# Optimization experiments

Hardware: AMD Instinct MI355X
Metric: run time of the kernel (lower is better)

## Reference

```python
import jax, jax.numpy as jnp
import numpy as np

K, B, T, Y, X, HY, HX = 8, 64, 128, 128, 64, 256, 256


def sparsemax(z):
    # projection onto the simplex along last axis
    zs = jnp.flip(jnp.sort(z, axis=-1), axis=-1)
    k = jnp.arange(1, z.shape[-1] + 1, dtype=z.dtype)
    cssv = jnp.cumsum(zs, axis=-1) - 1.0
    cond = k * zs > cssv
    kz = jnp.sum(cond, axis=-1, keepdims=True)
    tau = jnp.take_along_axis(cssv, kz - 1, axis=-1) / kz.astype(z.dtype)
    return jnp.maximum(z - tau, 0.0)


def rnn_relu(x, Wih, Whh, bih, bhh, h0):
    # batch-first relu RNN: x [B,T,D] -> h [B,T,H]
    xW = jnp.einsum('btd,hd->bth', x, Wih) + bih
    h0b = jnp.broadcast_to(h0, (x.shape[0], h0.shape[0]))
    def step(h, xt):
        h = jax.nn.relu(xt + h @ Whh.T + bhh)
        return h, h
    _, hs = jax.lax.scan(step, h0b, jnp.swapaxes(xW, 0, 1))
    return jnp.swapaxes(hs, 0, 1)


def setup_inputs() -> dict:
    ks = jax.random.split(jax.random.key(0), 32)
    s = 0.05
    p = lambda k, sh: jax.random.normal(k, sh, jnp.float32) * s
    return {
        'data': jax.random.normal(ks[0], (B, T, Y), jnp.float32),
        'eps_qx': jax.random.normal(ks[1], (K, B, T, X), jnp.float32),
        'eps_z': jax.random.normal(ks[2], (T, B, K), jnp.float32),
        'eps_x': jax.random.normal(ks[3], (T, B, X), jnp.float32),
        'y_Wih': p(ks[4], (K, HY, Y)), 'y_Whh': p(ks[5], (K, HY, HY)),
        'y_bih': p(ks[6], (K, HY)), 'y_bhh': p(ks[7], (K, HY)),
        'y_h0': jnp.zeros((K, HY), jnp.float32),
        'y_Wmu': p(ks[8], (K, X, HY)), 'y_bmu': p(ks[9], (K, X)),
        'x_Wih': p(ks[10], (K, HX, X)), 'x_Whh': p(ks[11], (K, HX, HX)),
        'x_bih': p(ks[12], (K, HX)), 'x_bhh': p(ks[13], (K, HX)),
        'x_h0': jnp.zeros((K, HX), jnp.float32),
        'ds_W': p(ks[14], (HX, K * HX)), 'ds_b': p(ks[15], (HX,)),
        'cb_W1': p(ks[16], (HX, K)), 'cb_b1': p(ks[17], (HX,)),
        'cb_W2': p(ks[18], (K, HX)), 'cb_b2': p(ks[19], (K,)),
        'z_q0': jnp.zeros((K,), jnp.float32),
    }


def _forward(data, eps_qx, eps_z, eps_x, y_Wih, y_Whh, y_bih, y_bhh, y_h0,
             y_Wmu, y_bmu, x_Wih, x_Whh, x_bih, x_bhh, x_h0,
             ds_W, ds_b, cb_W1, cb_b1, cb_W2, cb_b2, z_q0):
    Bn, Tn, _ = data.shape
    Kn = z_q0.shape[0]
    vr = jax.vmap(rnn_relu, in_axes=(None, 0, 0, 0, 0, 0))
    vrx = jax.vmap(rnn_relu, in_axes=(0, 0, 0, 0, 0, 0))
    # per-state LDM inference over reversed y: q(x^k_{1:T} | y_{1:T})
    data_rev = jnp.flip(data, axis=1)
    h_y = jnp.flip(vr(data_rev, y_Wih, y_Whh, y_bih, y_bhh, y_h0), axis=2)  # [K,B,T,HY]
    q_x_mu = jnp.einsum('kbth,kxh->kbtx', h_y, y_Wmu) + y_bmu[:, None, None, :]
    q_x_logvar = jnp.zeros_like(q_x_mu)
    q_x = q_x_mu + eps_qx  # sigma = exp(0.5*0) = 1
    # per-state summary RNN over reversed q_x samples
    q_x_rev = jnp.flip(q_x, axis=2)
    h_x = jnp.flip(vrx(q_x_rev, x_Wih, x_Whh, x_bih, x_bhh, x_h0), axis=2)  # [K,B,T,HX]
    summary = jnp.transpose(h_x, (1, 2, 0, 3)).reshape(Bn, Tn, -1)  # [B,T,K*HX]
    xs = summary @ ds_W.T + ds_b  # downsampler -> [B,T,HX]
    xs_t_all = jnp.swapaxes(xs, 0, 1)              # [T,B,HX]
    mu_t_all = jnp.transpose(q_x_mu, (2, 1, 0, 3))  # [T,B,K,X]
    z0 = jnp.broadcast_to(z_q0, (Bn, Kn))
    def step(z_prev, inp):
        xs_t, mu_t, ez, ex = inp
        h = z_prev @ cb_W1.T + cb_b1 + xs_t          # combiner hidden
        z_mu = h @ cb_W2.T + cb_b2                   # logits mu (logvar=0)
        z_t = z_mu + ez
        w = sparsemax(z_t)                            # [B,K] gating
        x_t = jnp.einsum('bk,bkx->bx', w, mu_t) + ex  # mixture reparam (sigma=1)
        return z_t, (x_t, z_t, z_mu)
    _, (x_s, z_s, z_l) = jax.lax.scan(step, z0, (xs_t_all, mu_t_all, eps_z, eps_x))
    x_sample = jnp.swapaxes(x_s, 0, 1)
    z_sample = jnp.swapaxes(z_s, 0, 1)
    z_logits = jnp.swapaxes(z_l, 0, 1)
    return (x_sample, q_x_mu, q_x_logvar, z_sample, z_logits)


def reference(data, eps_qx, eps_z, eps_x, y_Wih, y_Whh, y_bih, y_bhh, y_h0,
              y_Wmu, y_bmu, x_Wih, x_Whh, x_bih, x_bhh, x_h0,
              ds_W, ds_b, cb_W1, cb_b1, cb_W2, cb_b2, z_q0):
    return _forward(data, eps_qx, eps_z, eps_x, y_Wih, y_Whh, y_bih, y_bhh, y_h0,
                    y_Wmu, y_bmu, x_Wih, x_Whh, x_bih, x_bhh, x_h0,
                    ds_W, ds_b, cb_W1, cb_b1, cb_W2, cb_b2, z_q0)
```

## Files before the change

### kernel.cpp

```cpp
#include <hip/hip_runtime.h>

#define Kc 8
#define Bc 64
#define Tc 128
#define Yc 128
#define Xc 64
#define Hc 256
#define Rc 8192

typedef unsigned short u16;
typedef unsigned int u32;
typedef __attribute__((ext_vector_type(8))) short short8;
typedef __attribute__((ext_vector_type(4))) float f32x4;
typedef __attribute__((ext_vector_type(2))) unsigned int u32x2;

#define OFF_DATA 0L
#define OFF_YWIH 1048576L
#define OFF_YWHH 1310720L
#define OFF_YWMU 1835008L
#define OFF_XWIH 1966080L
#define OFF_XWHH 2097152L
#define OFF_M2   2621440L
#define OFF_QXF  2654208L
#define OFF_BUF1 6848512L
#define U16_BYTES 80805888L
#define FO_YB 0L
#define FO_XB 2048L
#define FO_CB 4096L
#define FO_A2 4112L
#define FO_CP 8192L
#define FO_C  532480L
#define FO_W  598016L


#define O_XS  0L
#define O_QMU 524288L
#define O_QLV 4718592L
#define O_ZS  8912896L
#define O_ZL  8978432L

__device__ __forceinline__ u16 f2bf(float f) {
  union { float f; u32 u; } v; v.f = f;
  u32 u = v.u;
  return (u16)((u + 0x7FFFu + ((u >> 16) & 1u)) >> 16);
}
__device__ __forceinline__ float bitsf(u32 u) {
  union { u32 u; float f; } v; v.u = u; return v.f;
}
__device__ __forceinline__ u32 cvt_pk(float lo, float hi) {
  u32 r;
  asm("v_cvt_pk_bf16_f32 %0, %1, %2" : "=v"(r) : "v"(lo), "v"(hi));
  return r;
}
__device__ __forceinline__ f32x4 mfma16(short8 a, short8 b, f32x4 c) {
  return __builtin_amdgcn_mfma_f32_16x16x32_bf16(a, b, c, 0, 0, 0);
}

__global__ void k_prep(const float* __restrict__ data, const float* __restrict__ yWih,
                       const float* __restrict__ yWhh, const float* __restrict__ yWmu,
                       const float* __restrict__ xWih, const float* __restrict__ xWhh,
                       const float* __restrict__ ybih, const float* __restrict__ ybhh,
                       const float* __restrict__ xbih, const float* __restrict__ xbhh,
                       u16* __restrict__ W, float* __restrict__ F, float* __restrict__ out)
{
  long tid = (long)blockIdx.x * blockDim.x + threadIdx.x;
  long stride = (long)gridDim.x * blockDim.x;
  for (long i = tid; i < 1048576L; i += stride) W[OFF_DATA + i] = f2bf(data[i]);
  for (long i = tid; i < 262144L;  i += stride) W[OFF_YWIH + i] = f2bf(yWih[i]);
  for (long i = tid; i < 524288L;  i += stride) W[OFF_YWHH + i] = f2bf(yWhh[i]);
  for (long i = tid; i < 131072L;  i += stride) W[OFF_YWMU + i] = f2bf(yWmu[i]);
  for (long i = tid; i < 131072L;  i += stride) W[OFF_XWIH + i] = f2bf(xWih[i]);
  for (long i = tid; i < 524288L;  i += stride) W[OFF_XWHH + i] = f2bf(xWhh[i]);
  for (long i = tid; i < 2048L;    i += stride) F[FO_YB + i] = ybih[i] + ybhh[i];
  for (long i = tid; i < 2048L;    i += stride) F[FO_XB + i] = xbih[i] + xbhh[i];
  for (long i = tid; i < 4194304L; i += stride) out[O_QLV + i] = 0.0f;
}

__global__ void k_prep2(const float* __restrict__ dsW, const float* __restrict__ dsb,
                        const float* __restrict__ W1, const float* __restrict__ b1,
                        const float* __restrict__ W2, const float* __restrict__ b2,
                        u16* __restrict__ W, float* __restrict__ F)
{
  if (blockIdx.x < 128) {
    long i = (long)blockIdx.x * 256 + threadIdx.x;
    int k2 = (int)(i >> 11), ki = (int)(i & 2047);
    float s = 0.0f;
    if (k2 < 8) {
      for (int j = 0; j < 256; ++j) s += W2[k2 * 256 + j] * dsW[(long)j * 2048 + ki];
    }
    W[OFF_M2 + i] = f2bf(s);
  } else {
    int t = threadIdx.x;
    if (t < 64) {
      int k2 = t >> 3, k1 = t & 7;
      float s = 0.0f;
      for (int j = 0; j < 256; ++j) s += W2[k2 * 256 + j] * W1[j * 8 + k1];
      F[FO_A2 + t] = s;
    } else if (t < 80) {
      int k2 = t - 64;
      float s = 0.0f;
      if (k2 < 8) {
        for (int j = 0; j < 256; ++j) s += W2[k2 * 256 + j] * (dsb[j] + b1[j]);
        s += b2[k2];
      }
      F[FO_CB + k2] = s;
    }
  }
}

__global__ __launch_bounds__(256) void k_g1(const u16* __restrict__ W, const float* __restrict__ F,
                                            u16* __restrict__ buf)
{
  const int k = blockIdx.y, bs = blockIdx.x >> 5, t0 = (blockIdx.x & 31) * 4;
  const int tid = threadIdx.x, wv = tid >> 6, l = tid & 63, lr = l & 15, lk = l >> 4;
  const int b0 = bs * 16;
  short8 Af[4][4];
  const u16* Ak = W + OFF_YWIH + (long)k * 32768;
#pragma unroll
  for (int nt = 0; nt < 4; ++nt)
#pragma unroll
    for (int kk = 0; kk < 4; ++kk)
      Af[nt][kk] = *(const short8*)(Ak + (long)(wv * 64 + nt * 16 + lr) * 128 + kk * 32 + lk * 8);
  f32x4 bias[4];
#pragma unroll
  for (int nt = 0; nt < 4; ++nt)
    bias[nt] = *(const f32x4*)&F[FO_YB + k * 256 + wv * 64 + nt * 16 + lk * 4];
  int roff[4];
#pragma unroll
  for (int nt = 0; nt < 4; ++nt)
    roff[nt] = (wv * 2 + (nt >> 1)) * 512 + ((nt & 1) * 2 + (lk >> 1)) * 128 + lr * 8 + (lk & 1) * 4;

  for (int ti = 0; ti < 4; ++ti) {
    int t = t0 + ti;
    f32x4 acc[4] = {bias[0], bias[1], bias[2], bias[3]};
    const u16* Brow = W + OFF_DATA + ((long)(b0 + lr) * 128 + t) * 128 + lk * 8;
#pragma unroll
    for (int kk = 0; kk < 4; ++kk) {
      short8 b = *(const short8*)(Brow + kk * 32);
      acc[0] = mfma16(Af[0][kk], b, acc[0]);
      acc[1] = mfma16(Af[1][kk], b, acc[1]);
      acc[2] = mfma16(Af[2][kk], b, acc[2]);
      acc[3] = mfma16(Af[3][kk], b, acc[3]);
    }
    u16* tb = buf + ((long)(k * 4 + bs) * 128 + t) * 4096;
#pragma unroll
    for (int nt = 0; nt < 4; ++nt) {
      u32 d0 = cvt_pk(acc[nt][0], acc[nt][1]);
      u32 d1 = cvt_pk(acc[nt][2], acc[nt][3]);
      *(u32x2*)(tb + roff[nt]) = (u32x2){d0, d1};
    }
  }
}

#define RNNY_STEP(T_, XW_, PIN_, POUT_)                                       \
  {                                                                           \
    f32x4 acc[4];                                                             \
    _Pragma("unroll")                                                         \
    for (int nt = 0; nt < 4; ++nt) {                                          \
      u32 w0 = XW_[nt * 2], w1 = XW_[nt * 2 + 1];                             \
      acc[nt][0] = bitsf(w0 << 16);                                           \
      acc[nt][1] = bitsf(w0 & 0xffff0000u);                                   \
      acc[nt][2] = bitsf(w1 << 16);                                           \
      acc[nt][3] = bitsf(w1 & 0xffff0000u);                                   \
    }                                                                         \
    if ((T_) >= 2) {                                                          \
      _Pragma("unroll")                                                       \
      for (int nt = 0; nt < 4; ++nt) {                                        \
        u32x2 v = *(const u32x2*)(tb0 + (long)((T_) - 2) * 4096 + roff[nt]);  \
        XW_[nt * 2] = v.x; XW_[nt * 2 + 1] = v.y;                             \
      }                                                                       \
    }                                                                         \
    _Pragma("unroll")                                                         \
    for (int kk = 0; kk < 8; ++kk) {                                          \
      short8 b = *(const short8*)&hlds[PIN_][kk * 512 + fro];                 \
      acc[0] = mfma16(Bf[0][kk], b, acc[0]);                                  \
      acc[1] = mfma16(Bf[1][kk], b, acc[1]);                                  \
      acc[2] = mfma16(Bf[2][kk], b, acc[2]);                                  \
      acc[3] = mfma16(Bf[3][kk], b, acc[3]);                                  \
    }                                                                         \
    u16* tb = tb0 + (long)(T_) * 4096;                                        \
    _Pragma("unroll")                                                         \
    for (int nt = 0; nt < 4; ++nt) {                                          \
      float f0 = fmaxf(acc[nt][0], 0.0f), f1 = fmaxf(acc[nt][1], 0.0f);       \
      float f2 = fmaxf(acc[nt][2], 0.0f), f3 = fmaxf(acc[nt][3], 0.0f);       \
      u32x2 d = (u32x2){cvt_pk(f0, f1), cvt_pk(f2, f3)};                      \
      *(u32x2*)&hlds[POUT_][roff[nt]] = d;                                    \
      *(u32x2*)(tb + roff[nt]) = d;                                           \
    }                                                                         \
    asm volatile("s_waitcnt lgkmcnt(0)" ::: "memory");                        \
    __builtin_amdgcn_s_barrier();                                             \
    __builtin_amdgcn_sched_barrier(0);                                        \
  }

__global__ __launch_bounds__(256, 1) void k_rnnY(u16* __restrict__ buf,
                                                 const u16* __restrict__ Whh,
                                                 const float* __restrict__ h0)
{
  const int k = blockIdx.y, bs = blockIdx.x;
  const int tid = threadIdx.x, wv = tid >> 6, l = tid & 63, lr = l & 15, lk = l >> 4;
  const int fro = lk * 128 + lr * 8;
  __shared__ __align__(16) u16 hlds[2][4096];

  short8 Bf[4][8];
  const u16* Wk = Whh + (long)k * 65536;
#pragma unroll
  for (int nt = 0; nt < 4; ++nt)
#pragma unroll
    for (int kk = 0; kk < 8; ++kk)
      Bf[nt][kk] = *(const short8*)(Wk + (long)(wv * 64 + nt * 16 + lr) * 256 + kk * 32 + lk * 8);

  for (int i = tid; i < 4096; i += 256) {
    int n = (i >> 9) * 32 + ((i >> 7) & 3) * 8 + (i & 7);
    hlds[0][i] = f2bf(h0[k * 256 + n]);
  }

  u16* tb0 = buf + (long)(k * 4 + bs) * 128 * 4096;
  int roff[4];
#pragma unroll
  for (int nt = 0; nt < 4; ++nt)
    roff[nt] = (wv * 2 + (nt >> 1)) * 512 + ((nt & 1) * 2 + (lk >> 1)) * 128 + lr * 8 + (lk & 1) * 4;

  u32 xwA[8], xwB[8];
#pragma unroll
  for (int nt = 0; nt < 4; ++nt) {
    u32x2 vA = *(const u32x2*)(tb0 + (long)(Tc - 1) * 4096 + roff[nt]);
    xwA[nt * 2] = vA.x; xwA[nt * 2 + 1] = vA.y;
    u32x2 vB = *(const u32x2*)(tb0 + (long)(Tc - 2) * 4096 + roff[nt]);
    xwB[nt * 2] = vB.x; xwB[nt * 2 + 1] = vB.y;
  }
  __syncthreads();

  for (int t = Tc - 1; t >= 1; t -= 2) {
    RNNY_STEP(t, xwA, 0, 1);
    RNNY_STEP(t - 1, xwB, 1, 0);
  }
}

__global__ __launch_bounds__(256) void k_g2(const u16* __restrict__ W, const u16* __restrict__ hy,
                                            const float* __restrict__ bmu, const float* __restrict__ eps,
                                            float* __restrict__ out, u16* __restrict__ qxf)
{
  const int k = blockIdx.y, bs = blockIdx.x >> 5, t0 = (blockIdx.x & 31) * 4;
  const int tid = threadIdx.x, wv = tid >> 6, l = tid & 63, lr = l & 15, lk = l >> 4;
  const int b0 = bs * 16, x0 = wv * 16;
  short8 Af[8];
  const u16* Ak = W + OFF_YWMU + (long)k * 16384;
#pragma unroll
  for (int kk = 0; kk < 8; ++kk)
    Af[kk] = *(const short8*)(Ak + (long)(x0 + lr) * 256 + kk * 32 + lk * 8);
  f32x4 bias = *(const f32x4*)&bmu[k * 64 + x0 + lk * 4];
  const int qoff = (wv >> 1) * 512 + ((wv & 1) * 2 + (lk >> 1)) * 128 + lr * 8 + (lk & 1) * 4;

  for (int ti = 0; ti < 4; ++ti) {
    int t = t0 + ti;
    const u16* tb = hy + ((long)(k * 4 + bs) * 128 + t) * 4096 + lk * 128 + lr * 8;
    f32x4 a0 = bias, a1 = (f32x4){0.f, 0.f, 0.f, 0.f};
#pragma unroll
    for (int kk = 0; kk < 8; kk += 2) {
      short8 bA = *(const short8*)(tb + kk * 512);
      short8 bB = *(const short8*)(tb + (kk + 1) * 512);
      a0 = mfma16(Af[kk], bA, a0);
      a1 = mfma16(Af[kk + 1], bB, a1);
    }
    f32x4 mu = a0 + a1;
    long idx = ((long)k * Rc + (b0 + lr) * 128 + t) * 64 + x0 + lk * 4;
    *(f32x4*)&out[O_QMU + idx] = mu;
    f32x4 e = *(const f32x4*)&eps[idx];
    f32x4 q = mu + e;
    *(u32x2*)(qxf + ((long)(k * 4 + bs) * 128 + t) * 1024 + qoff) =
        (u32x2){cvt_pk(q[0], q[1]), cvt_pk(q[2], q[3])};
  }
}

#define RNNX_STEP(T_, QC_, PIN_, POUT_)                                       \
  {                                                                           \
    short8 q0 = QC_[0], q1 = QC_[1];                                          \
    if ((T_) >= 2) {                                                          \
      QC_[0] = *(const short8*)(qb0 + (long)((T_) - 2) * 1024 + fro);         \
      QC_[1] = *(const short8*)(qb0 + (long)((T_) - 2) * 1024 + 512 + fro);   \
    }                                                                         \
    f32x4 acc[4] = {xbias[0], xbias[1], xbias[2], xbias[3]};                  \
    f32x4 cacc = (f32x4){0.f, 0.f, 0.f, 0.f};                                 \
    _Pragma("unroll")                                                         \
    for (int kk = 0; kk < 8; ++kk) {                                          \
      short8 b = *(const short8*)&hlds[PIN_][kk * 512 + fro];                 \
      acc[0] = mfma16(Bf[0][kk], b, acc[0]);                                  \
      acc[1] = mfma16(Bf[1][kk], b, acc[1]);                                  \
      acc[2] = mfma16(Bf[2][kk], b, acc[2]);                                  \
      acc[3] = mfma16(Bf[3][kk], b, acc[3]);                                  \
      if (wv == 0) cacc = mfma16(Mf[kk], b, cacc);                            \
    }                                                                         \
    acc[0] = mfma16(IhX[0][0], q0, acc[0]);                                   \
    acc[1] = mfma16(IhX[1][0], q0, acc[1]);                                   \
    acc[2] = mfma16(IhX[2][0], q0, acc[2]);                                   \
    acc[3] = mfma16(IhX[3][0], q0, acc[3]);                                   \
    acc[0] = mfma16(IhX[0][1], q1, acc[0]);                                   \
    acc[1] = mfma16(IhX[1][1], q1, acc[1]);                                   \
    acc[2] = mfma16(IhX[2][1], q1, acc[2]);                                   \
    acc[3] = mfma16(IhX[3][1], q1, acc[3]);                                   \
    if (wv == 0 && (T_) < Tc - 1 && lk < 2)                                   \
      *(f32x4*)&cp[((long)(b0 + lr) * Tc + (T_) + 1) * 8 + lk * 4] = cacc;    \
    _Pragma("unroll")                                                         \
    for (int nt = 0; nt < 4; ++nt) {                                          \
      float f0 = fmaxf(acc[nt][0], 0.0f), f1 = fmaxf(acc[nt][1], 0.0f);       \
      float f2 = fmaxf(acc[nt][2], 0.0f), f3 = fmaxf(acc[nt][3], 0.0f);       \
      *(u32x2*)&hlds[POUT_][roff[nt]] = (u32x2){cvt_pk(f0, f1), cvt_pk(f2, f3)}; \
    }                                                                         \
    asm volatile("s_waitcnt lgkmcnt(0)" ::: "memory");                        \
    __builtin_amdgcn_s_barrier();                                             \
    __builtin_amdgcn_sched_barrier(0);                                        \
  }

__global__ __launch_bounds__(256, 1) void k_rnnX(const u16* __restrict__ W,
                                                 const float* __restrict__ F,
                                                 const u16* __restrict__ qxf,
                                                 const float* __restrict__ h0,
                                                 float* __restrict__ cpart)
{
  const int k = blockIdx.y, bs = blockIdx.x, b0 = bs * 16;
  const int tid = threadIdx.x, wv = tid >> 6, l = tid & 63, lr = l & 15, lk = l >> 4;
  const int fro = lk * 128 + lr * 8;
  __shared__ __align__(16) u16 hlds[2][4096];

  short8 Bf[4][8];
  short8 IhX[4][2];
  short8 Mf[8];
  {
    const u16* Wk = W + OFF_XWHH + (long)k * 65536;
    const u16* Ik = W + OFF_XWIH + (long)k * 16384;
    const u16* Mk = W + OFF_M2 + (long)k * 256;
#pragma unroll
    for (int nt = 0; nt < 4; ++nt) {
#pragma unroll
      for (int kk = 0; kk < 8; ++kk)
        Bf[nt][kk] = *(const short8*)(Wk + (long)(wv * 64 + nt * 16 + lr) * 256 + kk * 32 + lk * 8);
#pragma unroll
      for (int kk = 0; kk < 2; ++kk)
        IhX[nt][kk] = *(const short8*)(Ik + (long)(wv * 64 + nt * 16 + lr) * 64 + kk * 32 + lk * 8);
    }
#pragma unroll
    for (int kk = 0; kk < 8; ++kk)
      Mf[kk] = *(const short8*)(Mk + (long)lr * 2048 + kk * 32 + lk * 8);
  }
  f32x4 xbias[4];
#pragma unroll
  for (int nt = 0; nt < 4; ++nt)
    xbias[nt] = *(const f32x4*)&F[FO_XB + k * 256 + wv * 64 + nt * 16 + lk * 4];
  int roff[4];
#pragma unroll
  for (int nt = 0; nt < 4; ++nt)
    roff[nt] = (wv * 2 + (nt >> 1)) * 512 + ((nt & 1) * 2 + (lk >> 1)) * 128 + lr * 8 + (lk & 1) * 4;

  for (int i = tid; i < 4096; i += 256) {
    int n = (i >> 9) * 32 + ((i >> 7) & 3) * 8 + (i & 7);
    hlds[0][i] = f2bf(h0[k * 256 + n]);
  }

  const u16* qb0 = qxf + (long)(k * 4 + bs) * 128 * 1024;
  float* cp = cpart + (long)k * Rc * 8;

  short8 qA[2], qB[2];
#pragma unroll
  for (int kk = 0; kk < 2; ++kk) {
    qA[kk] = *(const short8*)(qb0 + (long)(Tc - 1) * 1024 + kk * 512 + fro);
    qB[kk] = *(const short8*)(qb0 + (long)(Tc - 2) * 1024 + kk * 512 + fro);
  }
  __syncthreads();

  for (int t = Tc - 1; t >= 1; t -= 2) {
    RNNX_STEP(t, qA, 0, 1);
    RNNX_STEP(t - 1, qB, 1, 0);
  }
  if (wv == 0) {
    f32x4 cacc = (f32x4){0.f, 0.f, 0.f, 0.f};
#pragma unroll
    for (int kk = 0; kk < 8; ++kk) {
      short8 b = *(const short8*)&hlds[0][kk * 512 + fro];
      cacc = mfma16(Mf[kk], b, cacc);
    }
    if (lk < 2)
      *(f32x4*)&cp[((long)(b0 + lr) * Tc) * 8 + lk * 4] = cacc;
  }
}

__global__ void k_csum(const float* __restrict__ cpart, const float* __restrict__ F,
                       float* __restrict__ cbuf)
{
  int i = blockIdx.x * 256 + threadIdx.x;
  float s = F[FO_CB + (i & 7)];
#pragma unroll
  for (int k = 0; k < 8; ++k) s += cpart[(long)k * 65536 + i];
  cbuf[i] = s;
}

#define CASD(a, b) { float _hi = fmaxf(a, b), _lo = fminf(a, b); a = _hi; b = _lo; }
__global__ __launch_bounds__(256) void k_zchain(const float* __restrict__ F, const float* __restrict__ cbuf,
                                                const float* __restrict__ eps_z, const float* __restrict__ zq0,
                                                float* __restrict__ out, float* __restrict__ wbuf)
{
  const int wv = threadIdx.x >> 6, l = threadIdx.x & 63;
  const int b = blockIdx.x * 4 + wv;
  __shared__ float cl[4][1024];
  __shared__ float el[4][1024];
  for (int i = l; i < 1024; i += 64) cl[wv][i] = cbuf[(long)b * 1024 + i];
  for (int i = l; i < 1024; i += 64) {
    int t = i >> 3, kk = i & 7;
    el[wv][i] = eps_z[(long)t * (Bc * Kc) + b * 8 + kk];
  }
  float a2 = F[FO_A2 + l];
  __syncthreads();

  float z = zq0[l & 7];
  for (int t = 0; t < Tc; ++t) {
    float p = a2 * z;
    p += __shfl_xor(p, 1, 64);
    p += __shfl_xor(p, 2, 64);
    p += __shfl_xor(p, 4, 64);
    float zmu_l = __shfl(p, (l & 7) * 8, 64);
    float zl = zmu_l + cl[wv][t * 8 + (l & 7)];
    float zt = zl + el[wv][t * 8 + (l & 7)];

    float v0 = __shfl(zt, 0, 64), v1 = __shfl(zt, 1, 64), v2 = __shfl(zt, 2, 64), v3 = __shfl(zt, 3, 64);
    float v4 = __shfl(zt, 4, 64), v5 = __shfl(zt, 5, 64), v6 = __shfl(zt, 6, 64), v7 = __shfl(zt, 7, 64);
    CASD(v0, v1); CASD(v2, v3); CASD(v4, v5); CASD(v6, v7);
    CASD(v0, v2); CASD(v1, v3); CASD(v4, v6); CASD(v5, v7);
    CASD(v1, v2); CASD(v5, v6);
    CASD(v0, v4); CASD(v1, v5); CASD(v2, v6); CASD(v3, v7);
    CASD(v2, v4); CASD(v3, v5);
    CASD(v1, v2); CASD(v3, v4); CASD(v5, v6);
    float s0 = v0, s1 = s0 + v1, s2 = s1 + v2, s3 = s2 + v3;
    float s4 = s3 + v4, s5 = s4 + v5, s6 = s5 + v6, s7 = s6 + v7;
    int kz = 1;
    kz += (2.0f * v1 > s1 - 1.0f) ? 1 : 0;
    kz += (3.0f * v2 > s2 - 1.0f) ? 1 : 0;
    kz += (4.0f * v3 > s3 - 1.0f) ? 1 : 0;
    kz += (5.0f * v4 > s4 - 1.0f) ? 1 : 0;
    kz += (6.0f * v5 > s5 - 1.0f) ? 1 : 0;
    kz += (7.0f * v6 > s6 - 1.0f) ? 1 : 0;
    kz += (8.0f * v7 > s7 - 1.0f) ? 1 : 0;
    float csel = s0 - 1.0f;
    csel = (kz > 1) ? s1 - 1.0f : csel;
    csel = (kz > 2) ? s2 - 1.0f : csel;
    csel = (kz > 3) ? s3 - 1.0f : csel;
    csel = (kz > 4) ? s4 - 1.0f : csel;
    csel = (kz > 5) ? s5 - 1.0f : csel;
    csel = (kz > 6) ? s6 - 1.0f : csel;
    csel = (kz > 7) ? s7 - 1.0f : csel;
    float tau = csel / (float)kz;
    float wk = fmaxf(zt - tau, 0.0f);

    if (l < 8) {
      long r = (long)b * Tc + t;
      out[O_ZL + r * 8 + l] = zl;
      out[O_ZS + r * 8 + l] = zt;
      wbuf[r * 8 + l] = wk;
    }
    z = zt;
  }
}

__global__ void k_xsample(const float* __restrict__ wbuf, const float* __restrict__ eps_x,
                          float* __restrict__ out)
{
  long idx = (long)blockIdx.x * 256 + threadIdx.x;
  if (idx >= (long)Rc * Xc) return;
  long r = idx >> 6;
  int x = (int)(idx & 63);
  long b = r >> 7;
  long t = r & 127;
  float s = eps_x[(t * Bc + b) * 64 + x];
#pragma unroll
  for (int k = 0; k < 8; ++k)
    s += wbuf[r * 8 + k] * out[O_QMU + ((long)k * Rc + r) * 64 + x];
  out[O_XS + idx] = s;
}

extern "C" void kernel_launch(void* const* d_in, const int* in_sizes, int n_in,
                              void* d_out, int out_size, void* d_ws, size_t ws_size,
                              hipStream_t stream) {
  (void)in_sizes; (void)n_in; (void)out_size; (void)ws_size;
  const float* data   = (const float*)d_in[0];
  const float* eps_qx = (const float*)d_in[1];
  const float* eps_z  = (const float*)d_in[2];
  const float* eps_x  = (const float*)d_in[3];
  const float* yWih   = (const float*)d_in[4];
  const float* yWhh   = (const float*)d_in[5];
  const float* ybih   = (const float*)d_in[6];
  const float* ybhh   = (const float*)d_in[7];
  const float* yh0    = (const float*)d_in[8];
  const float* yWmu   = (const float*)d_in[9];
  const float* ybmu   = (const float*)d_in[10];
  const float* xWih   = (const float*)d_in[11];
  const float* xWhh   = (const float*)d_in[12];
  const float* xbih   = (const float*)d_in[13];
  const float* xbhh   = (const float*)d_in[14];
  const float* xh0    = (const float*)d_in[15];
  const float* dsW    = (const float*)d_in[16];
  const float* dsb    = (const float*)d_in[17];
  const float* cbW1   = (const float*)d_in[18];
  const float* cbb1   = (const float*)d_in[19];
  const float* cbW2   = (const float*)d_in[20];
  const float* cbb2   = (const float*)d_in[21];
  const float* zq0    = (const float*)d_in[22];

  u16*   W = (u16*)d_ws;
  float* F = (float*)((char*)d_ws + U16_BYTES);
  float* out = (float*)d_out;

  hipLaunchKernelGGL(k_prep, dim3(1024), dim3(256), 0, stream,
                     data, yWih, yWhh, yWmu, xWih, xWhh, ybih, ybhh, xbih, xbhh, W, F, out);
  hipLaunchKernelGGL(k_prep2, dim3(129), dim3(256), 0, stream,
                     dsW, dsb, cbW1, cbb1, cbW2, cbb2, W, F);
  hipLaunchKernelGGL(k_g1, dim3(128, 8), dim3(256), 0, stream, W, F, W + OFF_BUF1);
  hipLaunchKernelGGL(k_rnnY, dim3(4, 8), dim3(256), 0, stream, W + OFF_BUF1, W + OFF_YWHH, yh0);
  hipLaunchKernelGGL(k_g2, dim3(128, 8), dim3(256), 0, stream,
                     W, W + OFF_BUF1, ybmu, eps_qx, out, W + OFF_QXF);
  hipLaunchKernelGGL(k_rnnX, dim3(4, 8), dim3(256), 0, stream,
                     W, F, W + OFF_QXF, xh0, F + FO_CP);
  hipLaunchKernelGGL(k_csum, dim3(256), dim3(256), 0, stream, F + FO_CP, F, F + FO_C);
  hipLaunchKernelGGL(k_zchain, dim3(16), dim3(256), 0, stream, F, F + FO_C, eps_z, zq0, out, F + FO_W);
  hipLaunchKernelGGL(k_xsample, dim3(2048), dim3(256), 0, stream, F + FO_W, eps_x, out);
}
```

Measured before the change: 328.6 us.

## Use 8 waves per block in recurrent RNN kernels and fuse csum into zchain

Both sequential RNN kernels now run 512 threads (8 waves) per block, and each wave owns 32 hidden units instead of 64. That halves the MFMA chain each wave issues per serial timestep, which shortens the latency-bound recurrence. The separate k_csum kernel is removed and its partial-sum reduction is folded into k_zchain's load phase, saving one launch. In exchange there are more waves in each barrier, and the zchain prologue does more global reads.

```diff
diff --git a/kernel.cpp b/kernel.cpp
--- a/kernel.cpp
+++ b/kernel.cpp
@@ -29,7 +29,6 @@
 #define FO_CB 4096L
 #define FO_A2 4112L
 #define FO_CP 8192L
-#define FO_C  532480L
 #define FO_W  598016L
 
 
@@ -154,45 +153,37 @@
 
 #define RNNY_STEP(T_, XW_, PIN_, POUT_)                                       \
   {                                                                           \
-    f32x4 acc[4];                                                             \
-    _Pragma("unroll")                                                         \
-    for (int nt = 0; nt < 4; ++nt) {                                          \
-      u32 w0 = XW_[nt * 2], w1 = XW_[nt * 2 + 1];                             \
-      acc[nt][0] = bitsf(w0 << 16);                                           \
-      acc[nt][1] = bitsf(w0 & 0xffff0000u);                                   \
-      acc[nt][2] = bitsf(w1 << 16);                                           \
-      acc[nt][3] = bitsf(w1 & 0xffff0000u);                                   \
-    }                                                                         \
+    f32x4 acc0, acc1;                                                         \
+    { u32 w0 = XW_[0], w1 = XW_[1];                                           \
+      acc0[0] = bitsf(w0 << 16); acc0[1] = bitsf(w0 & 0xffff0000u);           \
+      acc0[2] = bitsf(w1 << 16); acc0[3] = bitsf(w1 & 0xffff0000u); }         \
+    { u32 w0 = XW_[2], w1 = XW_[3];                                           \
+      acc1[0] = bitsf(w0 << 16); acc1[1] = bitsf(w0 & 0xffff0000u);           \
+      acc1[2] = bitsf(w1 << 16); acc1[3] = bitsf(w1 & 0xffff0000u); }         \
     if ((T_) >= 2) {                                                          \
-      _Pragma("unroll")                                                       \
-      for (int nt = 0; nt < 4; ++nt) {                                        \
-        u32x2 v = *(const u32x2*)(tb0 + (long)((T_) - 2) * 4096 + roff[nt]);  \
-        XW_[nt * 2] = v.x; XW_[nt * 2 + 1] = v.y;                             \
-      }                                                                       \
+      u32x2 v0 = *(const u32x2*)(tb0 + (long)((T_) - 2) * 4096 + roff[0]);    \
+      u32x2 v1 = *(const u32x2*)(tb0 + (long)((T_) - 2) * 4096 + roff[1]);    \
+      XW_[0] = v0.x; XW_[1] = v0.y; XW_[2] = v1.x; XW_[3] = v1.y;             \
     }                                                                         \
     _Pragma("unroll")                                                         \
     for (int kk = 0; kk < 8; ++kk) {                                          \
       short8 b = *(const short8*)&hlds[PIN_][kk * 512 + fro];                 \
-      acc[0] = mfma16(Bf[0][kk], b, acc[0]);                                  \
-      acc[1] = mfma16(Bf[1][kk], b, acc[1]);                                  \
-      acc[2] = mfma16(Bf[2][kk], b, acc[2]);                                  \
-      acc[3] = mfma16(Bf[3][kk], b, acc[3]);                                  \
+      acc0 = mfma16(Bf[0][kk], b, acc0);                                      \
+      acc1 = mfma16(Bf[1][kk], b, acc1);                                      \
     }                                                                         \
     u16* tb = tb0 + (long)(T_) * 4096;                                        \
-    _Pragma("unroll")                                                         \
-    for (int nt = 0; nt < 4; ++nt) {                                          \
-      float f0 = fmaxf(acc[nt][0], 0.0f), f1 = fmaxf(acc[nt][1], 0.0f);       \
-      float f2 = fmaxf(acc[nt][2], 0.0f), f3 = fmaxf(acc[nt][3], 0.0f);       \
-      u32x2 d = (u32x2){cvt_pk(f0, f1), cvt_pk(f2, f3)};                      \
-      *(u32x2*)&hlds[POUT_][roff[nt]] = d;                                    \
-      *(u32x2*)(tb + roff[nt]) = d;                                           \
-    }                                                                         \
+    { u32x2 d = (u32x2){cvt_pk(fmaxf(acc0[0], 0.f), fmaxf(acc0[1], 0.f)),     \
+                        cvt_pk(fmaxf(acc0[2], 0.f), fmaxf(acc0[3], 0.f))};    \
+      *(u32x2*)&hlds[POUT_][roff[0]] = d; *(u32x2*)(tb + roff[0]) = d; }      \
+    { u32x2 d = (u32x2){cvt_pk(fmaxf(acc1[0], 0.f), fmaxf(acc1[1], 0.f)),     \
+                        cvt_pk(fmaxf(acc1[2], 0.f), fmaxf(acc1[3], 0.f))};    \
+      *(u32x2*)&hlds[POUT_][roff[1]] = d; *(u32x2*)(tb + roff[1]) = d; }      \
     asm volatile("s_waitcnt lgkmcnt(0)" ::: "memory");                        \
     __builtin_amdgcn_s_barrier();                                             \
     __builtin_amdgcn_sched_barrier(0);                                        \
   }
 
-__global__ __launch_bounds__(256, 1) void k_rnnY(u16* __restrict__ buf,
+__global__ __launch_bounds__(512, 1) void k_rnnY(u16* __restrict__ buf,
                                                  const u16* __restrict__ Whh,
                                                  const float* __restrict__ h0)
 {
@@ -201,32 +192,33 @@
   const int fro = lk * 128 + lr * 8;
   __shared__ __align__(16) u16 hlds[2][4096];
 
-  short8 Bf[4][8];
+  short8 Bf[2][8];
   const u16* Wk = Whh + (long)k * 65536;
 #pragma unroll
-  for (int nt = 0; nt < 4; ++nt)
+  for (int nt = 0; nt < 2; ++nt)
 #pragma unroll
     for (int kk = 0; kk < 8; ++kk)
-      Bf[nt][kk] = *(const short8*)(Wk + (long)(wv * 64 + nt * 16 + lr) * 256 + kk * 32 + lk * 8);
-
-  for (int i = tid; i < 4096; i += 256) {
+      Bf[nt][kk] = *(const short8*)(Wk + (long)(wv * 32 + nt * 16 + lr) * 256 + kk * 32 + lk * 8);
+
+  for (int i = tid; i < 4096; i += 512) {
     int n = (i >> 9) * 32 + ((i >> 7) & 3) * 8 + (i & 7);
     hlds[0][i] = f2bf(h0[k * 256 + n]);
   }
 
   u16* tb0 = buf + (long)(k * 4 + bs) * 128 * 4096;
-  int roff[4];
-#pragma unroll
-  for (int nt = 0; nt < 4; ++nt)
-    roff[nt] = (wv * 2 + (nt >> 1)) * 512 + ((nt & 1) * 2 + (lk >> 1)) * 128 + lr * 8 + (lk & 1) * 4;
-
-  u32 xwA[8], xwB[8];
-#pragma unroll
-  for (int nt = 0; nt < 4; ++nt) {
-    u32x2 vA = *(const u32x2*)(tb0 + (long)(Tc - 1) * 4096 + roff[nt]);
-    xwA[nt * 2] = vA.x; xwA[nt * 2 + 1] = vA.y;
-    u32x2 vB = *(const u32x2*)(tb0 + (long)(Tc - 2) * 4096 + roff[nt]);
-    xwB[nt * 2] = vB.x; xwB[nt * 2 + 1] = vB.y;
+  int roff[2];
+#pragma unroll
+  for (int nt = 0; nt < 2; ++nt)
+    roff[nt] = wv * 512 + (nt * 2 + (lk >> 1)) * 128 + lr * 8 + (lk & 1) * 4;
+
+  u32 xwA[4], xwB[4];
+  {
+    u32x2 a0 = *(const u32x2*)(tb0 + (long)(Tc - 1) * 4096 + roff[0]);
+    u32x2 a1 = *(const u32x2*)(tb0 + (long)(Tc - 1) * 4096 + roff[1]);
+    xwA[0] = a0.x; xwA[1] = a0.y; xwA[2] = a1.x; xwA[3] = a1.y;
+    u32x2 b0v = *(const u32x2*)(tb0 + (long)(Tc - 2) * 4096 + roff[0]);
+    u32x2 b1v = *(const u32x2*)(tb0 + (long)(Tc - 2) * 4096 + roff[1]);
+    xwB[0] = b0v.x; xwB[1] = b0v.y; xwB[2] = b1v.x; xwB[3] = b1v.y;
   }
   __syncthreads();
 
@@ -279,39 +271,33 @@
       QC_[0] = *(const short8*)(qb0 + (long)((T_) - 2) * 1024 + fro);         \
       QC_[1] = *(const short8*)(qb0 + (long)((T_) - 2) * 1024 + 512 + fro);   \
     }                                                                         \
-    f32x4 acc[4] = {xbias[0], xbias[1], xbias[2], xbias[3]};                  \
+    f32x4 acc0 = xbias[0], acc1 = xbias[1];                                   \
     f32x4 cacc = (f32x4){0.f, 0.f, 0.f, 0.f};                                 \
     _Pragma("unroll")                                                         \
     for (int kk = 0; kk < 8; ++kk) {                                          \
       short8 b = *(const short8*)&hlds[PIN_][kk * 512 + fro];                 \
-      acc[0] = mfma16(Bf[0][kk], b, acc[0]);                                  \
-      acc[1] = mfma16(Bf[1][kk], b, acc[1]);                                  \
-      acc[2] = mfma16(Bf[2][kk], b, acc[2]);                                  \
-      acc[3] = mfma16(Bf[3][kk], b, acc[3]);                                  \
+      acc0 = mfma16(Bf[0][kk], b, acc0);                                      \
+      acc1 = mfma16(Bf[1][kk], b, acc1);                                      \
       if (wv == 0) cacc = mfma16(Mf[kk], b, cacc);                            \
     }                                                                         \
-    acc[0] = mfma16(IhX[0][0], q0, acc[0]);                                   \
-    acc[1] = mfma16(IhX[1][0], q0, acc[1]);                                   \
-    acc[2] = mfma16(IhX[2][0], q0, acc[2]);                                   \
-    acc[3] = mfma16(IhX[3][0], q0, acc[3]);                                   \
-    acc[0] = mfma16(IhX[0][1], q1, acc[0]);                                   \
-    acc[1] = mfma16(IhX[1][1], q1, acc[1]);                                   \
-    acc[2] = mfma16(IhX[2][1], q1, acc[2]);                                   \
-    acc[3] = mfma16(IhX[3][1], q1, acc[3]);                                   \
+    acc0 = mfma16(IhX[0][0], q0, acc0);                                       \
+    acc1 = mfma16(IhX[1][0], q0, acc1);                                       \
+    acc0 = mfma16(IhX[0][1], q1, acc0);                                       \
+    acc1 = mfma16(IhX[1][1], q1, acc1);                                       \
     if (wv == 0 && (T_) < Tc - 1 && lk < 2)                                   \
       *(f32x4*)&cp[((long)(b0 + lr) * Tc + (T_) + 1) * 8 + lk * 4] = cacc;    \
-    _Pragma("unroll")                                                         \
-    for (int nt = 0; nt < 4; ++nt) {                                          \
-      float f0 = fmaxf(acc[nt][0], 0.0f), f1 = fmaxf(acc[nt][1], 0.0f);       \
-      float f2 = fmaxf(acc[nt][2], 0.0f), f3 = fmaxf(acc[nt][3], 0.0f);       \
-      *(u32x2*)&hlds[POUT_][roff[nt]] = (u32x2){cvt_pk(f0, f1), cvt_pk(f2, f3)}; \
-    }                                                                         \
+    { u32x2 d = (u32x2){cvt_pk(fmaxf(acc0[0], 0.f), fmaxf(acc0[1], 0.f)),     \
+                        cvt_pk(fmaxf(acc0[2], 0.f), fmaxf(acc0[3], 0.f))};    \
+      *(u32x2*)&hlds[POUT_][roff[0]] = d; }                                   \
+    { u32x2 d = (u32x2){cvt_pk(fmaxf(acc1[0], 0.f), fmaxf(acc1[1], 0.f)),     \
+                        cvt_pk(fmaxf(acc1[2], 0.f), fmaxf(acc1[3], 0.f))};    \
+      *(u32x2*)&hlds[POUT_][roff[1]] = d; }                                   \
     asm volatile("s_waitcnt lgkmcnt(0)" ::: "memory");                        \
     __builtin_amdgcn_s_barrier();                                             \
     __builtin_amdgcn_sched_barrier(0);                                        \
   }
 
-__global__ __launch_bounds__(256, 1) void k_rnnX(const u16* __restrict__ W,
+__global__ __launch_bounds__(512, 1) void k_rnnX(const u16* __restrict__ W,
                                                  const float* __restrict__ F,
                                                  const u16* __restrict__ qxf,
                                                  const float* __restrict__ h0,
@@ -322,36 +308,36 @@
   const int fro = lk * 128 + lr * 8;
   __shared__ __align__(16) u16 hlds[2][4096];
 
-  short8 Bf[4][8];
-  short8 IhX[4][2];
+  short8 Bf[2][8];
+  short8 IhX[2][2];
   short8 Mf[8];
   {
     const u16* Wk = W + OFF_XWHH + (long)k * 65536;
     const u16* Ik = W + OFF_XWIH + (long)k * 16384;
     const u16* Mk = W + OFF_M2 + (long)k * 256;
 #pragma unroll
-    for (int nt = 0; nt < 4; ++nt) {
+    for (int nt = 0; nt < 2; ++nt) {
 #pragma unroll
       for (int kk = 0; kk < 8; ++kk)
-        Bf[nt][kk] = *(const short8*)(Wk + (long)(wv * 64 + nt * 16 + lr) * 256 + kk * 32 + lk * 8);
+        Bf[nt][kk] = *(const short8*)(Wk + (long)(wv * 32 + nt * 16 + lr) * 256 + kk * 32 + lk * 8);
 #pragma unroll
       for (int kk = 0; kk < 2; ++kk)
-        IhX[nt][kk] = *(const short8*)(Ik + (long)(wv * 64 + nt * 16 + lr) * 64 + kk * 32 + lk * 8);
+        IhX[nt][kk] = *(const short8*)(Ik + (long)(wv * 32 + nt * 16 + lr) * 64 + kk * 32 + lk * 8);
     }
 #pragma unroll
     for (int kk = 0; kk < 8; ++kk)
       Mf[kk] = *(const short8*)(Mk + (long)lr * 2048 + kk * 32 + lk * 8);
   }
-  f32x4 xbias[4];
-#pragma unroll
-  for (int nt = 0; nt < 4; ++nt)
-    xbias[nt] = *(const f32x4*)&F[FO_XB + k * 256 + wv * 64 + nt * 16 + lk * 4];
-  int roff[4];
-#pragma unroll
-  for (int nt = 0; nt < 4; ++nt)
-    roff[nt] = (wv * 2 + (nt >> 1)) * 512 + ((nt & 1) * 2 + (lk >> 1)) * 128 + lr * 8 + (lk & 1) * 4;
-
-  for (int i = tid; i < 4096; i += 256) {
+  f32x4 xbias[2];
+#pragma unroll
+  for (int nt = 0; nt < 2; ++nt)
+    xbias[nt] = *(const f32x4*)&F[FO_XB + k * 256 + wv * 32 + nt * 16 + lk * 4];
+  int roff[2];
+#pragma unroll
+  for (int nt = 0; nt < 2; ++nt)
+    roff[nt] = wv * 512 + (nt * 2 + (lk >> 1)) * 128 + lr * 8 + (lk & 1) * 4;
+
+  for (int i = tid; i < 4096; i += 512) {
     int n = (i >> 9) * 32 + ((i >> 7) & 3) * 8 + (i & 7);
     hlds[0][i] = f2bf(h0[k * 256 + n]);
   }
@@ -383,18 +369,8 @@
   }
 }
 
-__global__ void k_csum(const float* __restrict__ cpart, const float* __restrict__ F,
-                       float* __restrict__ cbuf)
-{
-  int i = blockIdx.x * 256 + threadIdx.x;
-  float s = F[FO_CB + (i & 7)];
-#pragma unroll
-  for (int k = 0; k < 8; ++k) s += cpart[(long)k * 65536 + i];
-  cbuf[i] = s;
-}
-
 #define CASD(a, b) { float _hi = fmaxf(a, b), _lo = fminf(a, b); a = _hi; b = _lo; }
-__global__ __launch_bounds__(256) void k_zchain(const float* __restrict__ F, const float* __restrict__ cbuf,
+__global__ __launch_bounds__(256) void k_zchain(const float* __restrict__ F, const float* __restrict__ cpart,
                                                 const float* __restrict__ eps_z, const float* __restrict__ zq0,
                                                 float* __restrict__ out, float* __restrict__ wbuf)
 {
@@ -402,7 +378,12 @@
   const int b = blockIdx.x * 4 + wv;
   __shared__ float cl[4][1024];
   __shared__ float el[4][1024];
-  for (int i = l; i < 1024; i += 64) cl[wv][i] = cbuf[(long)b * 1024 + i];
+  for (int i = l; i < 1024; i += 64) {
+    float s = F[FO_CB + (i & 7)];
+#pragma unroll
+    for (int kq = 0; kq < 8; ++kq) s += cpart[(long)kq * 65536 + (long)b * 1024 + i];
+    cl[wv][i] = s;
+  }
   for (int i = l; i < 1024; i += 64) {
     int t = i >> 3, kk = i & 7;
     el[wv][i] = eps_z[(long)t * (Bc * Kc) + b * 8 + kk];
@@ -512,12 +493,11 @@
   hipLaunchKernelGGL(k_prep2, dim3(129), dim3(256), 0, stream,
                      dsW, dsb, cbW1, cbb1, cbW2, cbb2, W, F);
   hipLaunchKernelGGL(k_g1, dim3(128, 8), dim3(256), 0, stream, W, F, W + OFF_BUF1);
-  hipLaunchKernelGGL(k_rnnY, dim3(4, 8), dim3(256), 0, stream, W + OFF_BUF1, W + OFF_YWHH, yh0);
+  hipLaunchKernelGGL(k_rnnY, dim3(4, 8), dim3(512), 0, stream, W + OFF_BUF1, W + OFF_YWHH, yh0);
   hipLaunchKernelGGL(k_g2, dim3(128, 8), dim3(256), 0, stream,
                      W, W + OFF_BUF1, ybmu, eps_qx, out, W + OFF_QXF);
-  hipLaunchKernelGGL(k_rnnX, dim3(4, 8), dim3(256), 0, stream,
+  hipLaunchKernelGGL(k_rnnX, dim3(4, 8), dim3(512), 0, stream,
                      W, F, W + OFF_QXF, xh0, F + FO_CP);
-  hipLaunchKernelGGL(k_csum, dim3(256), dim3(256), 0, stream, F + FO_CP, F, F + FO_C);
-  hipLaunchKernelGGL(k_zchain, dim3(16), dim3(256), 0, stream, F, F + FO_C, eps_z, zq0, out, F + FO_W);
+  hipLaunchKernelGGL(k_zchain, dim3(16), dim3(256), 0, stream, F, F + FO_CP, eps_z, zq0, out, F + FO_W);
   hipLaunchKernelGGL(k_xsample, dim3(2048), dim3(256), 0, stream, F + FO_W, eps_x, out);
 }
```

Result: faster. 284.6 us (-13.4%).
